# Performance work log

Hardware: AMD Instinct MI355X
Metric: run time of the kernel (lower is better)

The kernel has to match this reference:

```python
import jax, jax.numpy as jnp
import numpy as np

HEADS = 16
ROPE_BASE = 10000.0


def _rope(x):
    # x: [B, S, D]; rotate interleaved even/odd pairs across full D
    B, S, D = x.shape
    half = D // 2
    inv_freq = 1.0 / (ROPE_BASE ** (jnp.arange(half, dtype=jnp.float32) * 2.0 / D))
    ang = jnp.arange(S, dtype=jnp.float32)[:, None] * inv_freq[None, :]  # [S, half]
    cos, sin = jnp.cos(ang), jnp.sin(ang)
    xp = x.reshape(B, S, half, 2)
    xe, xo = xp[..., 0], xp[..., 1]
    re = xe * cos - xo * sin
    ro = xe * sin + xo * cos
    return jnp.stack([re, ro], axis=-1).reshape(B, S, D)


def setup_inputs() -> dict:
    key = jax.random.key(0)
    ks = jax.random.split(key, 7)
    B, S, D = 2, 2048, 1024
    sc = 1.0 / np.sqrt(D)
    return {
        "queries": jax.random.normal(ks[0], (B, S, D), jnp.float32),
        "keys": jax.random.normal(ks[1], (B, S, D), jnp.float32),
        "values": jax.random.normal(ks[2], (B, S, D), jnp.float32),
        "Wq": jax.random.normal(ks[3], (D, D), jnp.float32) * sc,
        "Wk": jax.random.normal(ks[4], (D, D), jnp.float32) * sc,
        "Wv": jax.random.normal(ks[5], (D, D), jnp.float32) * sc,
        "Wo": jax.random.normal(ks[6], (D, D), jnp.float32) * sc,
    }


def reference(queries, keys, values, Wq, Wk, Wv, Wo):
    B, S, D = queries.shape
    H = HEADS
    dk = D // H
    # bias-free linear projections (torch Linear: x @ W^T)
    q = _rope(queries @ Wq.T)
    k = _rope(keys @ Wk.T)
    v = _rope(values @ Wv.T)
    # split heads: [B, H, S, dk]
    q = q.reshape(B, S, H, dk).transpose(0, 2, 1, 3)
    k = k.reshape(B, S, H, dk).transpose(0, 2, 1, 3)
    v = v.reshape(B, S, H, dk).transpose(0, 2, 1, 3)
    scores = jnp.einsum("bhqd,bhkd->bhqk", q, k) / jnp.sqrt(jnp.float32(dk))
    attn = jax.nn.softmax(scores, axis=-1)
    ctx = jnp.einsum("bhqk,bhkd->bhqd", attn, v)  # [B, H, S, dk]
    z = ctx.transpose(0, 2, 1, 3).reshape(B, S, D)
    return z @ Wo.T
```

## Files before the change

### kernel.cpp

```cpp
#include <hip/hip_runtime.h>
#include <hip/hip_bf16.h>
#include <math.h>


typedef __attribute__((ext_vector_type(8))) short s8v;
typedef __attribute__((ext_vector_type(8))) __bf16 bf16x8;
typedef __attribute__((ext_vector_type(4))) float f32x4;
typedef __attribute__((ext_vector_type(16))) float f32x16;
typedef __attribute__((ext_vector_type(2))) unsigned u32x2;

__device__ inline unsigned short f2bf(float f) {
    unsigned u = __builtin_bit_cast(unsigned, f);
    u += 0x7FFFu + ((u >> 16) & 1u);
    return (unsigned short)(u >> 16);
}

__device__ inline unsigned pk_bf16(float a, float b) {
    __hip_bfloat162 h = __float22bfloat162_rn(float2{a, b});
    unsigned u;
    __builtin_memcpy(&u, &h, 4);
    return u;
}

__device__ inline f32x4 mfma16(s8v a, s8v b, f32x4 c) {
    return __builtin_amdgcn_mfma_f32_16x16x32_bf16(
        __builtin_bit_cast(bf16x8, a), __builtin_bit_cast(bf16x8, b), c, 0, 0, 0);
}

__device__ inline f32x16 mfma32(s8v a, s8v b, f32x16 c) {
    return __builtin_amdgcn_mfma_f32_32x32x16_bf16(
        __builtin_bit_cast(bf16x8, a), __builtin_bit_cast(bf16x8, b), c, 0, 0, 0);
}

struct CvtArgs {
    const float* s[7];
    unsigned short* d[7];
    int n4[7];
};

__global__ __launch_bounds__(256) void cvt_kernel(CvtArgs a) {
    const int which = blockIdx.y;
    const float4* __restrict__ src = (const float4*)a.s[which];
    unsigned short* __restrict__ dst = a.d[which];
    const int n4 = a.n4[which];
    for (int i = blockIdx.x * 256 + threadIdx.x; i < n4; i += gridDim.x * 256) {
        float4 v = src[i];
        uint2 o;
        o.x = pk_bf16(v.x, v.y);
        o.y = pk_bf16(v.z, v.w);
        *(uint2*)(dst + (size_t)i * 4) = o;
    }
}

__global__ __launch_bounds__(256) void rope_table_kernel(float* __restrict__ cosT,
                                                         float* __restrict__ sinT) {
    int i = blockIdx.x * 256 + threadIdx.x;
    int s = i >> 9, d2 = i & 511;
    float inv = exp2f((float)d2 * (-13.287712379549449f / 512.0f));
    float ang = (float)s * inv;
    float sn, cs;
    sincosf(ang, &sn, &cs);
    cosT[i] = cs;
    sinT[i] = sn;
}

struct GemmArgs {
    const unsigned short* A[3];
    const unsigned short* W[3];
    void* C[3];
    const float* cosT;
    const float* sinT;
    float scale[3];
};

template <bool ROPE>
__global__ __launch_bounds__(256) void gemm_bt(GemmArgs g) {
    constexpr int K = 1024, N = 1024;
    const int z = blockIdx.z;
    const unsigned short* __restrict__ A = g.A[z];
    const unsigned short* __restrict__ W = g.W[z];

    const int tid = threadIdx.x;
    const int lane = tid & 63, wid = tid >> 6;
    const int wr = wid >> 1, wc = wid & 1;
    const int row0 = blockIdx.x * 128, col0 = blockIdx.y * 128;
    const int lr = lane & 15, kofs = (lane >> 4) * 8;

    __shared__ __align__(16) unsigned short As[128][72];
    __shared__ __align__(16) unsigned short Ws[128][72];

    f32x4 acc[4][4] = {};

    const int srow = tid >> 3;
    const int schunk = (tid & 7) * 8;

    for (int k0 = 0; k0 < K; k0 += 64) {
        __syncthreads();
#pragma unroll
        for (int i = 0; i < 4; ++i) {
            int r = srow + i * 32;
            *(s8v*)(&As[r][schunk]) =
                *(const s8v*)(A + (size_t)(row0 + r) * K + k0 + schunk);
            *(s8v*)(&Ws[r][schunk]) =
                *(const s8v*)(W + (size_t)(col0 + r) * K + k0 + schunk);
        }
        __syncthreads();

        s8v af[2][4], bf[2][4];
#pragma unroll
        for (int ks = 0; ks < 2; ++ks) {
#pragma unroll
            for (int m = 0; m < 4; ++m)
                af[ks][m] = *(const s8v*)(&As[wr * 64 + m * 16 + lr][ks * 32 + kofs]);
#pragma unroll
            for (int n = 0; n < 4; ++n)
                bf[ks][n] = *(const s8v*)(&Ws[wc * 64 + n * 16 + lr][ks * 32 + kofs]);
        }
#pragma unroll
        for (int m = 0; m < 4; ++m)
#pragma unroll
            for (int n = 0; n < 4; ++n) {
                acc[m][n] = mfma16(af[0][m], bf[0][n], acc[m][n]);
                acc[m][n] = mfma16(af[1][m], bf[1][n], acc[m][n]);
            }
    }

    const int rbase = row0 + wr * 64 + ((lane >> 4) << 2);
    const int cbase = col0 + wc * 64 + lr;
    const float scale = g.scale[z];
#pragma unroll
    for (int m = 0; m < 4; ++m) {
#pragma unroll
        for (int n = 0; n < 4; ++n) {
            const int gc = cbase + n * 16;
#pragma unroll
            for (int r = 0; r < 4; ++r) {
                const int gr = rbase + m * 16 + r;
                float v = acc[m][n][r];
                if constexpr (ROPE) {
                    const int s = gr & 2047;
                    const int d2 = gc >> 1;
                    float cs = g.cosT[s * 512 + d2];
                    float sn = g.sinT[s * 512 + d2];
                    float partner = __shfl_xor(v, 1);
                    v = (v * cs + partner * ((lane & 1) ? sn : -sn)) * scale;
                    ((unsigned short*)g.C[z])[(size_t)gr * N + gc] = f2bf(v);
                } else {
                    ((float*)g.C[z])[(size_t)gr * N + gc] = v;
                }
            }
        }
    }
}

__global__ __launch_bounds__(256, 2) void attn_kernel(
    const unsigned short* __restrict__ Q,
    const unsigned short* __restrict__ Km,
    const unsigned short* __restrict__ Vm,
    unsigned short* __restrict__ ctx) {
    const int tid = threadIdx.x;
    const int lane = tid & 63;
    const int w = tid >> 6;
    const int hi = lane >> 5;
    const int lq = lane & 31;
    const int flat = blockIdx.x;
    const int vid = (flat & 7) * 64 + (flat >> 3);
    const int qt = vid & 15;
    const int bh = vid >> 4;
    const size_t base = (size_t)(bh >> 4) * 2048 * 1024;
    const int hcol = (bh & 15) * 64;
    const int q0 = qt * 128 + w * 32;

    __shared__ __align__(16) unsigned short Vt[2][64][66];

    const int vkey = tid >> 3;
    const int vc = tid & 7;

    const unsigned short* kpa = Km + base + (size_t)lq * 1024 + hcol + hi * 8;
    const unsigned short* kpb = kpa + 32 * 1024;
    const unsigned short* vst = Vm + base + (size_t)vkey * 1024 + hcol + vc * 8;

    s8v qf[4];
#pragma unroll
    for (int s = 0; s < 4; ++s)
        qf[s] = *(const s8v*)(Q + base + (size_t)(q0 + lq) * 1024 + hcol + s * 16 + hi * 8);

    s8v kfA[8], kfB[8];
#pragma unroll
    for (int i = 0; i < 8; ++i)
        kfA[i] = *(const s8v*)(((i >> 2) ? kpb : kpa) + (i & 3) * 16);
    {
        s8v v00 = *(const s8v*)vst;
        s8v v01 = *(const s8v*)(vst + 32 * 1024);
#pragma unroll
        for (int j = 0; j < 8; ++j) {
            Vt[0][vc * 8 + j][vkey] = (unsigned short)v00[j];
            Vt[0][vc * 8 + j][vkey + 32] = (unsigned short)v01[j];
        }
    }
    kpa += 65536; kpb += 65536; vst += 65536;
    __syncthreads();

    f32x16 accO0 = {}, accO1 = {};
    float lacc = 0.f;

#if __has_builtin(__builtin_amdgcn_permlane32_swap)
#define PK_SWAP(fi, a0, b0, a1, b1)                                             \
    {                                                                           \
        u32x2 ra_ = __builtin_amdgcn_permlane32_swap((a0), (b0), false, false); \
        u32x2 rb_ = __builtin_amdgcn_permlane32_swap((a1), (b1), false, false); \
        fi.x = (int)ra_[0]; fi.y = (int)rb_[0];                                 \
        fi.z = (int)ra_[1]; fi.w = (int)rb_[1];                                 \
    }
#else
#define PK_SWAP(fi, a0, b0, a1, b1)                                             \
    {                                                                           \
        unsigned own0 = hi ? (b0) : (a0);                                       \
        unsigned own1 = hi ? (b1) : (a1);                                       \
        unsigned snd0 = hi ? (a0) : (b0);                                       \
        unsigned snd1 = hi ? (a1) : (b1);                                       \
        unsigned rcv0 = (unsigned)__shfl_xor((int)snd0, 32);                    \
        unsigned rcv1 = (unsigned)__shfl_xor((int)snd1, 32);                    \
        fi.x = (int)(hi ? rcv0 : own0);                                         \
        fi.y = (int)(hi ? rcv1 : own1);                                         \
        fi.z = (int)(hi ? own0 : rcv0);                                         \
        fi.w = (int)(hi ? own1 : rcv1);                                         \
    }
#endif

#define ATTN_STEP(KT, CUR, KFC, KFN)                                            \
    {                                                                           \
        const int kt_ = (KT);                                                   \
        const bool pre_ = (kt_ + 64 < 2048);                                    \
        s8v vn0_, vn1_;                                                         \
        if (pre_) {                                                             \
              \
            vn0_ = *(const s8v*)vst;                                            \
            vn1_ = *(const s8v*)(vst + 32 * 1024);                              \
            __builtin_amdgcn_sched_barrier(0);                                  \
            _Pragma("unroll")                                                   \
            for (int i = 0; i < 8; ++i)                                         \
                KFN[i] = *(const s8v*)(((i >> 2) ? kpb : kpa) + (i & 3) * 16);  \
        }                                                                       \
                                                      \
        f32x16 s0 = {}, s1 = {};                                                \
        __builtin_amdgcn_s_setprio(1);                                          \
        _Pragma("unroll")                                                       \
        for (int s = 0; s < 4; ++s) {                                           \
            s0 = mfma32(KFC[s], qf[s], s0);                                     \
            s1 = mfma32(KFC[4 + s], qf[s], s1);                                 \
        }                                                                       \
        __builtin_amdgcn_s_setprio(0);                                          \
                                  \
        _Pragma("unroll")                                                       \
        for (int r = 0; r < 16; ++r) {                                          \
            s0[r] = exp2f(s0[r]);                                               \
            s1[r] = exp2f(s1[r]);                                               \
        }                                                                       \
        float t16[16];                                                          \
        _Pragma("unroll")                                                       \
        for (int r = 0; r < 16; ++r) t16[r] = s0[r] + s1[r];                    \
        _Pragma("unroll")                                                       \
        for (int r = 0; r < 8; ++r) t16[r] += t16[r + 8];                       \
        _Pragma("unroll")                                                       \
        for (int r = 0; r < 4; ++r) t16[r] += t16[r + 4];                       \
        lacc += (t16[0] + t16[1]) + (t16[2] + t16[3]);                          \
        unsigned w0[8], w1[8];                                                  \
        _Pragma("unroll")                                                       \
        for (int g = 0; g < 4; ++g) {                                           \
            const int rr = g * 4;                                               \
            w0[g] = pk_bf16(s0[rr], s0[rr + 1]);                                \
            w1[g] = pk_bf16(s0[rr + 2], s0[rr + 3]);                            \
        }                                                                       \
        _Pragma("unroll")                                                       \
        for (int g = 4; g < 8; ++g) {                                           \
            const int rr = (g - 4) * 4;                                         \
            w0[g] = pk_bf16(s1[rr], s1[rr + 1]);                                \
            w1[g] = pk_bf16(s1[rr + 2], s1[rr + 3]);                            \
        }                                                                       \
        s8v pf[4];                                                              \
        _Pragma("unroll")                                                       \
        for (int ks = 0; ks < 4; ++ks) {                                        \
            int4 fi;                                                            \
            PK_SWAP(fi, w0[2 * ks], w0[2 * ks + 1], w1[2 * ks], w1[2 * ks + 1]);\
            pf[ks] = __builtin_bit_cast(s8v, fi);                               \
        }                                                                       \
                      \
        if (pre_) {                                                             \
            _Pragma("unroll")                                                   \
            for (int j = 0; j < 8; ++j) {                                       \
                Vt[(CUR) ^ 1][vc * 8 + j][vkey] = (unsigned short)vn0_[j];      \
                Vt[(CUR) ^ 1][vc * 8 + j][vkey + 32] = (unsigned short)vn1_[j]; \
            }                                                                   \
        }                                                                       \
        asm volatile("s_waitcnt lgkmcnt(0)" ::: "memory");                      \
        __builtin_amdgcn_s_barrier();                                           \
        __builtin_amdgcn_sched_barrier(0);                                      \
                                        \
        __builtin_amdgcn_s_setprio(1);                                          \
        _Pragma("unroll")                                                       \
        for (int ks = 0; ks < 4; ++ks) {                                        \
            s8v vf0 = *(const s8v*)&Vt[CUR][lq][ks * 16 + hi * 8];              \
            s8v vf1 = *(const s8v*)&Vt[CUR][32 + lq][ks * 16 + hi * 8];         \
            accO0 = mfma32(vf0, pf[ks], accO0);                                 \
            accO1 = mfma32(vf1, pf[ks], accO1);                                 \
        }                                                                       \
        __builtin_amdgcn_s_setprio(0);                                          \
        kpa += 65536; kpb += 65536; vst += 65536;                               \
    }

    for (int kt = 0; kt < 2048; kt += 128) {
        ATTN_STEP(kt, 0, kfA, kfB);
        ATTN_STEP(kt + 64, 1, kfB, kfA);
    }
#undef ATTN_STEP
#undef PK_SWAP

    const float ltot = lacc + __shfl_xor(lacc, 32);
    const float rl = 1.0f / ltot;
    unsigned short* dst = ctx + base + (size_t)(q0 + lq) * 1024 + hcol;
#pragma unroll
    for (int r = 0; r < 16; ++r) {
        const int d = (r & 3) + 8 * (r >> 2) + 4 * hi;
        dst[d] = f2bf(accO0[r] * rl);
        dst[d + 32] = f2bf(accO1[r] * rl);
    }
}

extern "C" void kernel_launch(void* const* d_in, const int* in_sizes, int n_in,
                              void* d_out, int out_size, void* d_ws, size_t ws_size,
                              hipStream_t stream) {
    char* ws = (char*)d_ws;
    size_t off = 0;
    auto alloc = [&](size_t bytes) {
        void* p = ws + off;
        off += (bytes + 255) & ~(size_t)255;
        return p;
    };

    const size_t XB = (size_t)4096 * 1024 * 2;
    const size_t WB = (size_t)1024 * 1024 * 2;
    const size_t TB = (size_t)2048 * 512 * 4;

    unsigned short* Xb[3];
    for (int i = 0; i < 3; ++i) Xb[i] = (unsigned short*)alloc(XB);
    unsigned short* Wb[4];
    for (int i = 0; i < 4; ++i) Wb[i] = (unsigned short*)alloc(WB);
    unsigned short* Qb = (unsigned short*)alloc(XB);
    unsigned short* Kb = (unsigned short*)alloc(XB);
    unsigned short* Vb = (unsigned short*)alloc(XB);
    float* cosT = (float*)alloc(TB);
    float* sinT = (float*)alloc(TB);
    unsigned short* ctx = Xb[0];

    CvtArgs ca;
    unsigned short* dsts[7] = {Xb[0], Xb[1], Xb[2], Wb[0], Wb[1], Wb[2], Wb[3]};
    for (int i = 0; i < 7; ++i) {
        ca.s[i] = (const float*)d_in[i];
        ca.d[i] = dsts[i];
        ca.n4[i] = in_sizes[i] / 4;
    }
    cvt_kernel<<<dim3(1024, 7), 256, 0, stream>>>(ca);

    rope_table_kernel<<<4096, 256, 0, stream>>>(cosT, sinT);

    GemmArgs gp;
    gp.A[0] = Xb[0]; gp.A[1] = Xb[1]; gp.A[2] = Xb[2];
    gp.W[0] = Wb[0]; gp.W[1] = Wb[1]; gp.W[2] = Wb[2];
    gp.C[0] = Qb;    gp.C[1] = Kb;    gp.C[2] = Vb;
    gp.cosT = cosT;  gp.sinT = sinT;
    gp.scale[0] = 0.125f * 1.4426950408889634f;
    gp.scale[1] = 1.0f;
    gp.scale[2] = 1.0f;
    gemm_bt<true><<<dim3(32, 8, 3), 256, 0, stream>>>(gp);

    attn_kernel<<<512, 256, 0, stream>>>(Qb, Kb, Vb, ctx);

    GemmArgs go;
    go.A[0] = ctx;   go.A[1] = ctx;   go.A[2] = ctx;
    go.W[0] = Wb[3]; go.W[1] = Wb[3]; go.W[2] = Wb[3];
    go.C[0] = d_out; go.C[1] = d_out; go.C[2] = d_out;
    go.cosT = cosT;  go.sinT = sinT;
    go.scale[0] = 1.0f; go.scale[1] = 1.0f; go.scale[2] = 1.0f;
    gemm_bt<false><<<dim3(32, 8, 1), 256, 0, stream>>>(go);
}
```

Measured before the change: 173.8 us.

## Stage GEMM tiles via direct global-to-LDS loads and shrink output GEMM tile

The GEMM kernel now stages A and W tiles with global_load_lds (16-byte direct-to-LDS loads), which skips the register round trip. To fit the per-wave contiguous layout it drops the LDS row padding, which may add bank conflicts on the fragment reads. The kernel is templated on BM, and the output projection uses 64-row tiles with twice as many blocks for better CU occupancy. The rope table switches to range-reduced __sincosf, a fast intrinsic with slightly different accuracy.

```diff
diff --git a/kernel.cpp b/kernel.cpp
--- a/kernel.cpp
+++ b/kernel.cpp
@@ -31,6 +31,17 @@
     return __builtin_amdgcn_mfma_f32_32x32x16_bf16(
         __builtin_bit_cast(bf16x8, a), __builtin_bit_cast(bf16x8, b), c, 0, 0, 0);
 }
+
+#if __has_builtin(__builtin_amdgcn_global_load_lds)
+#define STAGE16(gsrc, lwavebase)                                                \
+    __builtin_amdgcn_global_load_lds(                                           \
+        (const __attribute__((address_space(1))) unsigned int*)(gsrc),          \
+        (__attribute__((address_space(3))) unsigned int*)(lwavebase), 16, 0, 0)
+#else
+#define STAGE16(gsrc, lwavebase)                                                \
+    { *(s8v*)((unsigned short*)(lwavebase) + (threadIdx.x & 63) * 8) =          \
+          *(const s8v*)(gsrc); }
+#endif
 
 struct CvtArgs {
     const float* s[7];
@@ -57,9 +68,11 @@
     int i = blockIdx.x * 256 + threadIdx.x;
     int s = i >> 9, d2 = i & 511;
     float inv = exp2f((float)d2 * (-13.287712379549449f / 512.0f));
-    float ang = (float)s * inv;
+    float rev = (float)s * inv * 0.15915494309189535f;
+    rev -= floorf(rev);
+    float ang = rev * 6.283185307179586f;
     float sn, cs;
-    sincosf(ang, &sn, &cs);
+    __sincosf(ang, &sn, &cs);
     cosT[i] = cs;
     sinT[i] = sn;
 }
@@ -73,51 +86,57 @@
     float scale[3];
 };
 
-template <bool ROPE>
+template <bool ROPE, int BM>
 __global__ __launch_bounds__(256) void gemm_bt(GemmArgs g) {
     constexpr int K = 1024, N = 1024;
+    constexpr int MR = BM / 32;
+    constexpr int AJ = BM * 8 / 256;
     const int z = blockIdx.z;
     const unsigned short* __restrict__ A = g.A[z];
     const unsigned short* __restrict__ W = g.W[z];
 
     const int tid = threadIdx.x;
-    const int lane = tid & 63, wid = tid >> 6;
-    const int wr = wid >> 1, wc = wid & 1;
-    const int row0 = blockIdx.x * 128, col0 = blockIdx.y * 128;
+    const int lane = tid & 63, wv = tid >> 6;
+    const int wrr = (wv >> 1) * (BM / 2);
+    const int wc = wv & 1;
+    const int row0 = blockIdx.x * BM, col0 = blockIdx.y * 128;
     const int lr = lane & 15, kofs = (lane >> 4) * 8;
 
-    __shared__ __align__(16) unsigned short As[128][72];
-    __shared__ __align__(16) unsigned short Ws[128][72];
-
-    f32x4 acc[4][4] = {};
-
-    const int srow = tid >> 3;
-    const int schunk = (tid & 7) * 8;
+    __shared__ __align__(16) unsigned short As[BM][64];
+    __shared__ __align__(16) unsigned short Ws[128][64];
+
+    f32x4 acc[MR][4] = {};
 
     for (int k0 = 0; k0 < K; k0 += 64) {
         __syncthreads();
 #pragma unroll
-        for (int i = 0; i < 4; ++i) {
-            int r = srow + i * 32;
-            *(s8v*)(&As[r][schunk]) =
-                *(const s8v*)(A + (size_t)(row0 + r) * K + k0 + schunk);
-            *(s8v*)(&Ws[r][schunk]) =
-                *(const s8v*)(W + (size_t)(col0 + r) * K + k0 + schunk);
+        for (int j = 0; j < AJ; ++j) {
+            const int cib = j * 256 + wv * 64;
+            const int ci = cib + lane;
+            STAGE16(A + (size_t)(row0 + (ci >> 3)) * K + k0 + (ci & 7) * 8,
+                    &As[0][0] + (size_t)cib * 8);
+        }
+#pragma unroll
+        for (int j = 0; j < 4; ++j) {
+            const int cib = j * 256 + wv * 64;
+            const int ci = cib + lane;
+            STAGE16(W + (size_t)(col0 + (ci >> 3)) * K + k0 + (ci & 7) * 8,
+                    &Ws[0][0] + (size_t)cib * 8);
         }
         __syncthreads();
 
-        s8v af[2][4], bf[2][4];
+        s8v af[2][MR], bf[2][4];
 #pragma unroll
         for (int ks = 0; ks < 2; ++ks) {
 #pragma unroll
-            for (int m = 0; m < 4; ++m)
-                af[ks][m] = *(const s8v*)(&As[wr * 64 + m * 16 + lr][ks * 32 + kofs]);
+            for (int m = 0; m < MR; ++m)
+                af[ks][m] = *(const s8v*)(&As[wrr + m * 16 + lr][ks * 32 + kofs]);
 #pragma unroll
             for (int n = 0; n < 4; ++n)
                 bf[ks][n] = *(const s8v*)(&Ws[wc * 64 + n * 16 + lr][ks * 32 + kofs]);
         }
 #pragma unroll
-        for (int m = 0; m < 4; ++m)
+        for (int m = 0; m < MR; ++m)
 #pragma unroll
             for (int n = 0; n < 4; ++n) {
                 acc[m][n] = mfma16(af[0][m], bf[0][n], acc[m][n]);
@@ -125,11 +144,11 @@
             }
     }
 
-    const int rbase = row0 + wr * 64 + ((lane >> 4) << 2);
+    const int rbase = row0 + wrr + ((lane >> 4) << 2);
     const int cbase = col0 + wc * 64 + lr;
     const float scale = g.scale[z];
 #pragma unroll
-    for (int m = 0; m < 4; ++m) {
+    for (int m = 0; m < MR; ++m) {
 #pragma unroll
         for (int n = 0; n < 4; ++n) {
             const int gc = cbase + n * 16;
@@ -234,7 +253,6 @@
         const bool pre_ = (kt_ + 64 < 2048);                                    \
         s8v vn0_, vn1_;                                                         \
         if (pre_) {                                                             \
-              \
             vn0_ = *(const s8v*)vst;                                            \
             vn1_ = *(const s8v*)(vst + 32 * 1024);                              \
             __builtin_amdgcn_sched_barrier(0);                                  \
@@ -242,7 +260,6 @@
             for (int i = 0; i < 8; ++i)                                         \
                 KFN[i] = *(const s8v*)(((i >> 2) ? kpb : kpa) + (i & 3) * 16);  \
         }                                                                       \
-                                                      \
         f32x16 s0 = {}, s1 = {};                                                \
         __builtin_amdgcn_s_setprio(1);                                          \
         _Pragma("unroll")                                                       \
@@ -251,7 +268,6 @@
             s1 = mfma32(KFC[4 + s], qf[s], s1);                                 \
         }                                                                       \
         __builtin_amdgcn_s_setprio(0);                                          \
-                                  \
         _Pragma("unroll")                                                       \
         for (int r = 0; r < 16; ++r) {                                          \
             s0[r] = exp2f(s0[r]);                                               \
@@ -285,7 +301,6 @@
             PK_SWAP(fi, w0[2 * ks], w0[2 * ks + 1], w1[2 * ks], w1[2 * ks + 1]);\
             pf[ks] = __builtin_bit_cast(s8v, fi);                               \
         }                                                                       \
-                      \
         if (pre_) {                                                             \
             _Pragma("unroll")                                                   \
             for (int j = 0; j < 8; ++j) {                                       \
@@ -296,7 +311,6 @@
         asm volatile("s_waitcnt lgkmcnt(0)" ::: "memory");                      \
         __builtin_amdgcn_s_barrier();                                           \
         __builtin_amdgcn_sched_barrier(0);                                      \
-                                        \
         __builtin_amdgcn_s_setprio(1);                                          \
         _Pragma("unroll")                                                       \
         for (int ks = 0; ks < 4; ++ks) {                                        \
@@ -372,7 +386,7 @@
     gp.scale[0] = 0.125f * 1.4426950408889634f;
     gp.scale[1] = 1.0f;
     gp.scale[2] = 1.0f;
-    gemm_bt<true><<<dim3(32, 8, 3), 256, 0, stream>>>(gp);
+    gemm_bt<true, 128><<<dim3(32, 8, 3), 256, 0, stream>>>(gp);
 
     attn_kernel<<<512, 256, 0, stream>>>(Qb, Kb, Vb, ctx);
 
@@ -382,5 +396,5 @@
     go.C[0] = d_out; go.C[1] = d_out; go.C[2] = d_out;
     go.cosT = cosT;  go.sinT = sinT;
     go.scale[0] = 1.0f; go.scale[1] = 1.0f; go.scale[2] = 1.0f;
-    gemm_bt<false><<<dim3(32, 8, 1), 256, 0, stream>>>(go);
-}
+    gemm_bt<false, 64><<<dim3(64, 8, 1), 256, 0, stream>>>(go);
+}
```

Result: slower. 178.3 us (+2.6%).

## Split attention KV range across two wave groups and combine partial sums

Applied to the files above, without the earlier changes.

Doubles the attention block to 512 threads, with two groups of four waves each handling half of the key/value sequence for the same query tile, then merges the partial outputs and row sums through shared memory. It removes the register double-buffered K prefetch and the V double buffer, replacing them with a simple load-then-compute loop with two block barriers per step. The aim is more waves in flight to hide latency, at the cost of losing the software pipelining and adding a combine stage. Launch bounds change to 512 threads with 4 blocks per CU, which tightens the register budget.

```diff
diff --git a/kernel.cpp b/kernel.cpp
--- a/kernel.cpp
+++ b/kernel.cpp
@@ -153,7 +153,7 @@
     }
 }
 
-__global__ __launch_bounds__(256, 2) void attn_kernel(
+__global__ __launch_bounds__(512, 4) void attn_kernel(
     const unsigned short* __restrict__ Q,
     const unsigned short* __restrict__ Km,
     const unsigned short* __restrict__ Vm,
@@ -161,6 +161,8 @@
     const int tid = threadIdx.x;
     const int lane = tid & 63;
     const int w = tid >> 6;
+    const int h = w >> 2;
+    const int wp = w & 3;
     const int hi = lane >> 5;
     const int lq = lane & 31;
     const int flat = blockIdx.x;
@@ -169,37 +171,23 @@
     const int bh = vid >> 4;
     const size_t base = (size_t)(bh >> 4) * 2048 * 1024;
     const int hcol = (bh & 15) * 64;
-    const int q0 = qt * 128 + w * 32;
+    const int q0 = qt * 128 + wp * 32;
+    const int kv0 = h * 1024;
 
     __shared__ __align__(16) unsigned short Vt[2][64][66];
-
-    const int vkey = tid >> 3;
+    __shared__ __align__(16) float comb[4][64][33];
+
+    const int vkey = (tid & 255) >> 3;
     const int vc = tid & 7;
 
-    const unsigned short* kpa = Km + base + (size_t)lq * 1024 + hcol + hi * 8;
+    const unsigned short* kpa = Km + base + (size_t)(kv0 + lq) * 1024 + hcol + hi * 8;
     const unsigned short* kpb = kpa + 32 * 1024;
-    const unsigned short* vst = Vm + base + (size_t)vkey * 1024 + hcol + vc * 8;
+    const unsigned short* vst = Vm + base + (size_t)(kv0 + vkey) * 1024 + hcol + vc * 8;
 
     s8v qf[4];
 #pragma unroll
     for (int s = 0; s < 4; ++s)
         qf[s] = *(const s8v*)(Q + base + (size_t)(q0 + lq) * 1024 + hcol + s * 16 + hi * 8);
-
-    s8v kfA[8], kfB[8];
-#pragma unroll
-    for (int i = 0; i < 8; ++i)
-        kfA[i] = *(const s8v*)(((i >> 2) ? kpb : kpa) + (i & 3) * 16);
-    {
-        s8v v00 = *(const s8v*)vst;
-        s8v v01 = *(const s8v*)(vst + 32 * 1024);
-#pragma unroll
-        for (int j = 0; j < 8; ++j) {
-            Vt[0][vc * 8 + j][vkey] = (unsigned short)v00[j];
-            Vt[0][vc * 8 + j][vkey + 32] = (unsigned short)v01[j];
-        }
-    }
-    kpa += 65536; kpb += 65536; vst += 65536;
-    __syncthreads();
 
     f32x16 accO0 = {}, accO1 = {};
     float lacc = 0.f;
@@ -228,102 +216,99 @@
     }
 #endif
 
-#define ATTN_STEP(KT, CUR, KFC, KFN)                                            \
-    {                                                                           \
-        const int kt_ = (KT);                                                   \
-        const bool pre_ = (kt_ + 64 < 2048);                                    \
-        s8v vn0_, vn1_;                                                         \
-        if (pre_) {                                                             \
-              \
-            vn0_ = *(const s8v*)vst;                                            \
-            vn1_ = *(const s8v*)(vst + 32 * 1024);                              \
-            __builtin_amdgcn_sched_barrier(0);                                  \
-            _Pragma("unroll")                                                   \
-            for (int i = 0; i < 8; ++i)                                         \
-                KFN[i] = *(const s8v*)(((i >> 2) ? kpb : kpa) + (i & 3) * 16);  \
-        }                                                                       \
-                                                      \
-        f32x16 s0 = {}, s1 = {};                                                \
-        __builtin_amdgcn_s_setprio(1);                                          \
-        _Pragma("unroll")                                                       \
-        for (int s = 0; s < 4; ++s) {                                           \
-            s0 = mfma32(KFC[s], qf[s], s0);                                     \
-            s1 = mfma32(KFC[4 + s], qf[s], s1);                                 \
-        }                                                                       \
-        __builtin_amdgcn_s_setprio(0);                                          \
-                                  \
-        _Pragma("unroll")                                                       \
-        for (int r = 0; r < 16; ++r) {                                          \
-            s0[r] = exp2f(s0[r]);                                               \
-            s1[r] = exp2f(s1[r]);                                               \
-        }                                                                       \
-        float t16[16];                                                          \
-        _Pragma("unroll")                                                       \
-        for (int r = 0; r < 16; ++r) t16[r] = s0[r] + s1[r];                    \
-        _Pragma("unroll")                                                       \
-        for (int r = 0; r < 8; ++r) t16[r] += t16[r + 8];                       \
-        _Pragma("unroll")                                                       \
-        for (int r = 0; r < 4; ++r) t16[r] += t16[r + 4];                       \
-        lacc += (t16[0] + t16[1]) + (t16[2] + t16[3]);                          \
-        unsigned w0[8], w1[8];                                                  \
-        _Pragma("unroll")                                                       \
-        for (int g = 0; g < 4; ++g) {                                           \
-            const int rr = g * 4;                                               \
-            w0[g] = pk_bf16(s0[rr], s0[rr + 1]);                                \
-            w1[g] = pk_bf16(s0[rr + 2], s0[rr + 3]);                            \
-        }                                                                       \
-        _Pragma("unroll")                                                       \
-        for (int g = 4; g < 8; ++g) {                                           \
-            const int rr = (g - 4) * 4;                                         \
-            w0[g] = pk_bf16(s1[rr], s1[rr + 1]);                                \
-            w1[g] = pk_bf16(s1[rr + 2], s1[rr + 3]);                            \
-        }                                                                       \
-        s8v pf[4];                                                              \
-        _Pragma("unroll")                                                       \
-        for (int ks = 0; ks < 4; ++ks) {                                        \
-            int4 fi;                                                            \
-            PK_SWAP(fi, w0[2 * ks], w0[2 * ks + 1], w1[2 * ks], w1[2 * ks + 1]);\
-            pf[ks] = __builtin_bit_cast(s8v, fi);                               \
-        }                                                                       \
-                      \
-        if (pre_) {                                                             \
-            _Pragma("unroll")                                                   \
-            for (int j = 0; j < 8; ++j) {                                       \
-                Vt[(CUR) ^ 1][vc * 8 + j][vkey] = (unsigned short)vn0_[j];      \
-                Vt[(CUR) ^ 1][vc * 8 + j][vkey + 32] = (unsigned short)vn1_[j]; \
-            }                                                                   \
-        }                                                                       \
-        asm volatile("s_waitcnt lgkmcnt(0)" ::: "memory");                      \
-        __builtin_amdgcn_s_barrier();                                           \
-        __builtin_amdgcn_sched_barrier(0);                                      \
-                                        \
-        __builtin_amdgcn_s_setprio(1);                                          \
-        _Pragma("unroll")                                                       \
-        for (int ks = 0; ks < 4; ++ks) {                                        \
-            s8v vf0 = *(const s8v*)&Vt[CUR][lq][ks * 16 + hi * 8];              \
-            s8v vf1 = *(const s8v*)&Vt[CUR][32 + lq][ks * 16 + hi * 8];         \
-            accO0 = mfma32(vf0, pf[ks], accO0);                                 \
-            accO1 = mfma32(vf1, pf[ks], accO1);                                 \
-        }                                                                       \
-        __builtin_amdgcn_s_setprio(0);                                          \
-        kpa += 65536; kpb += 65536; vst += 65536;                               \
-    }
-
-    for (int kt = 0; kt < 2048; kt += 128) {
-        ATTN_STEP(kt, 0, kfA, kfB);
-        ATTN_STEP(kt + 64, 1, kfB, kfA);
-    }
-#undef ATTN_STEP
+    for (int st = 0; st < 16; ++st) {
+        s8v v00 = *(const s8v*)vst;
+        s8v v01 = *(const s8v*)(vst + 32 * 1024);
+        s8v kf[8];
+#pragma unroll
+        for (int i = 0; i < 8; ++i)
+            kf[i] = *(const s8v*)(((i >> 2) ? kpb : kpa) + (i & 3) * 16);
+#pragma unroll
+        for (int j = 0; j < 8; ++j) {
+            Vt[h][vc * 8 + j][vkey] = (unsigned short)v00[j];
+            Vt[h][vc * 8 + j][vkey + 32] = (unsigned short)v01[j];
+        }
+        f32x16 s0 = {}, s1 = {};
+        __builtin_amdgcn_s_setprio(1);
+#pragma unroll
+        for (int s = 0; s < 4; ++s) {
+            s0 = mfma32(kf[s], qf[s], s0);
+            s1 = mfma32(kf[4 + s], qf[s], s1);
+        }
+        __builtin_amdgcn_s_setprio(0);
+#pragma unroll
+        for (int r = 0; r < 16; ++r) {
+            s0[r] = exp2f(s0[r]);
+            s1[r] = exp2f(s1[r]);
+        }
+        float t16[16];
+#pragma unroll
+        for (int r = 0; r < 16; ++r) t16[r] = s0[r] + s1[r];
+#pragma unroll
+        for (int r = 0; r < 8; ++r) t16[r] += t16[r + 8];
+#pragma unroll
+        for (int r = 0; r < 4; ++r) t16[r] += t16[r + 4];
+        lacc += (t16[0] + t16[1]) + (t16[2] + t16[3]);
+        unsigned w0[8], w1[8];
+#pragma unroll
+        for (int g = 0; g < 4; ++g) {
+            const int rr = g * 4;
+            w0[g] = pk_bf16(s0[rr], s0[rr + 1]);
+            w1[g] = pk_bf16(s0[rr + 2], s0[rr + 3]);
+        }
+#pragma unroll
+        for (int g = 4; g < 8; ++g) {
+            const int rr = (g - 4) * 4;
+            w0[g] = pk_bf16(s1[rr], s1[rr + 1]);
+            w1[g] = pk_bf16(s1[rr + 2], s1[rr + 3]);
+        }
+        s8v pf[4];
+#pragma unroll
+        for (int ks = 0; ks < 4; ++ks) {
+            int4 fi;
+            PK_SWAP(fi, w0[2 * ks], w0[2 * ks + 1], w1[2 * ks], w1[2 * ks + 1]);
+            pf[ks] = __builtin_bit_cast(s8v, fi);
+        }
+        __syncthreads();
+        __builtin_amdgcn_s_setprio(1);
+#pragma unroll
+        for (int ks = 0; ks < 4; ++ks) {
+            s8v vf0 = *(const s8v*)&Vt[h][lq][ks * 16 + hi * 8];
+            s8v vf1 = *(const s8v*)&Vt[h][32 + lq][ks * 16 + hi * 8];
+            accO0 = mfma32(vf0, pf[ks], accO0);
+            accO1 = mfma32(vf1, pf[ks], accO1);
+        }
+        __builtin_amdgcn_s_setprio(0);
+        __syncthreads();
+        kpa += 65536; kpb += 65536; vst += 65536;
+    }
 #undef PK_SWAP
 
-    const float ltot = lacc + __shfl_xor(lacc, 32);
-    const float rl = 1.0f / ltot;
-    unsigned short* dst = ctx + base + (size_t)(q0 + lq) * 1024 + hcol;
-#pragma unroll
-    for (int r = 0; r < 16; ++r) {
-        const int d = (r & 3) + 8 * (r >> 2) + 4 * hi;
-        dst[d] = f2bf(accO0[r] * rl);
-        dst[d + 32] = f2bf(accO1[r] * rl);
+    if (h == 1) {
+#pragma unroll
+        for (int r = 0; r < 16; ++r) {
+            comb[wp][lane][r] = accO0[r];
+            comb[wp][lane][16 + r] = accO1[r];
+        }
+        comb[wp][lane][32] = lacc;
+    }
+    __syncthreads();
+    if (h == 0) {
+#pragma unroll
+        for (int r = 0; r < 16; ++r) {
+            accO0[r] += comb[wp][lane][r];
+            accO1[r] += comb[wp][lane][16 + r];
+        }
+        const float l2 = lacc + comb[wp][lane][32];
+        const float ltot = l2 + __shfl_xor(l2, 32);
+        const float rl = 1.0f / ltot;
+        unsigned short* dst = ctx + base + (size_t)(q0 + lq) * 1024 + hcol;
+#pragma unroll
+        for (int r = 0; r < 16; ++r) {
+            const int d = (r & 3) + 8 * (r >> 2) + 4 * hi;
+            dst[d] = f2bf(accO0[r] * rl);
+            dst[d + 32] = f2bf(accO1[r] * rl);
+        }
     }
 }
 
@@ -374,7 +359,7 @@
     gp.scale[2] = 1.0f;
     gemm_bt<true><<<dim3(32, 8, 3), 256, 0, stream>>>(gp);
 
-    attn_kernel<<<512, 256, 0, stream>>>(Qb, Kb, Vb, ctx);
+    attn_kernel<<<512, 512, 0, stream>>>(Qb, Kb, Vb, ctx);
 
     GemmArgs go;
     go.A[0] = ctx;   go.A[1] = ctx;   go.A[2] = ctx;
```

Result: faster. 162.1 us (-6.7%).
